# Optimization experiments

Measured on AMD Instinct MI355X. Metric: run time of the kernel, lower is better.

## Reference

```python
import jax, jax.numpy as jnp
from jax import lax
import numpy as np

N_HOS, N_TYPES, N_STRUCTS = 4, 16, 512
N_COMBOS = N_HOS * N_TYPES  # 64
HID = 1024
N_ITERS = 60  # fixed PDHG iterations (differentiable unrolled solver)


def setup_inputs() -> dict:
    key = jax.random.key(0)
    ks = jax.random.split(key, 8)
    X = jax.random.uniform(ks[0], (2048, N_HOS, N_TYPES), dtype=jnp.float32)
    # sparse 0/1 structure matrix; guarantee each structure touches >=1 combo
    S = (jax.random.uniform(ks[1], (N_COMBOS, N_STRUCTS)) < 0.08).astype(jnp.float32)
    cols = jnp.arange(N_STRUCTS)
    S = S.at[cols % N_COMBOS, cols].set(1.0)
    # MLP params (He-ish init)
    W1 = jax.random.normal(ks[2], (N_COMBOS, HID), dtype=jnp.float32) * (2.0 / N_COMBOS) ** 0.5
    b1 = jnp.zeros((HID,), jnp.float32)
    W2 = jax.random.normal(ks[3], (HID, HID), dtype=jnp.float32) * (2.0 / HID) ** 0.5
    b2 = jnp.zeros((HID,), jnp.float32)
    W3 = jax.random.normal(ks[4], (HID, N_STRUCTS), dtype=jnp.float32) * (2.0 / HID) ** 0.5
    b3 = jnp.zeros((N_STRUCTS,), jnp.float32)
    return {"X": X, "W1": W1, "b1": b1, "W2": W2, "b2": b2,
            "W3": W3, "b3": b3, "S": S, "batch_size": 2048}


def nn_forward(X, W1, b1, W2, b2, W3, b3):
    # torch loop applies act_fun after EVERY layer, including the last
    Z = X.reshape(X.shape[0], -1)                 # [B, n_hos*n_types]
    Z = jax.nn.relu(Z @ W1 + b1)
    Z = jax.nn.relu(Z @ W2 + b2)
    Z = jax.nn.relu(Z @ W3 + b3)                  # [B, n_structures]
    return Z


def solve_lp(S, W, B, Z, n_iters=N_ITERS):
    """Batched solve of: max_x W.x - ||x - Z||_2  s.t. x >= 0, S x <= B.
    PDHG (Chambolle-Pock) on  min_x f(x) + i{Kx <= c},
    f(x) = -W.x + ||x - Z||_2,  K = [S; -I],  c = [B; 0].
    Same optimization problem as the CvxpyLayer, solved by a fixed-iteration
    batched primal-dual method (differentiable via unrolling)."""
    batch, n = Z.shape
    m = S.shape[0]

    # ||K||_2 via power iteration on K^T K = S^T S + I (constant wrt params)
    def pow_step(v, _):
        v2 = S.T @ (S @ v) + v
        return v2 / jnp.linalg.norm(v2), None
    v0 = jnp.full((n,), 1.0 / np.sqrt(n), Z.dtype)
    v, _ = lax.scan(pow_step, v0, None, length=30)
    L = jnp.sqrt(jnp.vdot(v, S.T @ (S @ v) + v))
    L = lax.stop_gradient(L)
    tau = 0.9 / L
    sigma = 0.9 / L

    c = jnp.concatenate([B, jnp.zeros_like(Z)], axis=-1)  # [B, m+n]

    def Kx(x):
        return jnp.concatenate([x @ S.T, -x], axis=-1)    # [B, m+n]

    def KTy(y):
        return y[:, :m] @ S - y[:, m:]                    # [B, n]

    def prox_f(v):
        # argmin_x 1/(2 tau) ||x - v||^2 - W.x + ||x - Z||_2
        u = v + tau * W
        d = u - Z
        nrm = jnp.linalg.norm(d, axis=-1, keepdims=True)
        scale = jnp.maximum(1.0 - tau / jnp.maximum(nrm, 1e-12), 0.0)
        return Z + scale * d

    def step(carry, _):
        x, xbar, y = carry
        y = jnp.maximum(y + sigma * (Kx(xbar) - c), 0.0)
        x_new = prox_f(x - tau * KTy(y))
        xbar = 2.0 * x_new - x
        return (x_new, xbar, y), None

    x0 = jnp.zeros_like(Z)
    y0 = jnp.zeros((batch, m + n), Z.dtype)
    (x, _, _), _ = lax.scan(step, (x0, x0, y0), None, length=n_iters)
    return x


def reference(X, W1, b1, W2, b2, W3, b3, S, batch_size):
    Z = nn_forward(X, W1, b1, W2, b2, W3, b3)     # [B, n_structures]
    W = jnp.ones_like(Z)                          # weights w = 1 (as in torch)
    B = X.reshape(batch_size, -1)                 # capacities b
    return solve_lp(S, W, B, Z)
```

## Files before the change

kernel.cpp:

```cpp
#include <hip/hip_runtime.h>


typedef _Float16 half8 __attribute__((ext_vector_type(8)));
typedef __fp16 fp16x2 __attribute__((ext_vector_type(2)));
typedef __fp16 fp16x4 __attribute__((ext_vector_type(4)));
typedef float floatx4 __attribute__((ext_vector_type(4)));
typedef float floatx2 __attribute__((ext_vector_type(2)));

#define BATCH 2048
#define NITERS 60
#define XBS 520
#define YLS 72

typedef const __attribute__((address_space(1))) unsigned int* gptr_as1;
typedef __attribute__((address_space(3))) unsigned int* lptr_as3;
__device__ __forceinline__ void gl_lds16(const _Float16* g, _Float16* s) {
    __builtin_amdgcn_global_load_lds((gptr_as1)g, (lptr_as3)s, 16, 0, 0);
}

template <int CTRL>
__device__ __forceinline__ float dpp_addf(float x) {
    int y = __builtin_amdgcn_update_dpp(0, __builtin_bit_cast(int, x), CTRL, 0xf, 0xf, true);
    return x + __builtin_bit_cast(float, y);
}
__device__ __forceinline__ float sum16(float x) {
    x = dpp_addf<0xB1>(x);
    x = dpp_addf<0x4E>(x);
    x = dpp_addf<0x124>(x);
    x = dpp_addf<0x128>(x);
    return x;
}
__device__ __forceinline__ float sum64(float x) {
    x = sum16(x);
    x += __builtin_bit_cast(float, __builtin_amdgcn_ds_swizzle(__builtin_bit_cast(int, x), 0x401F));
    x += __shfl_xor(x, 32, 64);
    return x;
}

__device__ void power_64(const float* __restrict__ S, float* __restrict__ tau_g) {
    __shared__ unsigned long long rowm[64][8];
    __shared__ float G[64][65];
    __shared__ float wl[64], pg[4][64];
    int t = threadIdx.x, wv = t >> 6, ln = t & 63;
    for (int rr = 0; rr < 16; rr++) {
        int r = wv * 16 + rr;
        float v[8];
#pragma unroll
        for (int e = 0; e < 8; e++) v[e] = S[r * 512 + e * 64 + ln];
#pragma unroll
        for (int e = 0; e < 8; e++) {
            unsigned long long m = __ballot(v[e] != 0.f);
            if (ln == 0) rowm[r][e] = m;
        }
    }
    __syncthreads();
    for (int k = 0; k < 16; k++) {
        int idx = t * 16 + k;
        int i = idx >> 6, j = idx & 63;
        int cnt = 0;
#pragma unroll
        for (int e = 0; e < 8; e++) cnt += __popcll(rowm[i][e] & rowm[j][e]);
        G[i][j] = (float)cnt;
    }
    if (wv == 0) {
        int cnt = 0;
#pragma unroll
        for (int e = 0; e < 8; e++) cnt += __popcll(rowm[ln][e]);
        wl[ln] = (float)cnt * 0.044194173824159216f;
    }
    __syncthreads();
    for (int s = 0; s < 30; s++) {
        float a = 0.f;
#pragma unroll
        for (int jj = 0; jj < 16; jj++) {
            int j = wv * 16 + jj;
            a += G[ln][j] * wl[j];
        }
        pg[wv][ln] = a;
        __syncthreads();
        if (wv == 0) {
            float g = (pg[0][ln] + pg[1][ln]) + (pg[2][ln] + pg[3][ln]);
            float wi = wl[ln];
            float s1 = sum64(wi * g);
            float s2 = sum64(wi * wi);
            float n = sqrtf(s1 + 2.f * s2 + 1.f);
            wl[ln] = (g + wi) / n;
        }
        __syncthreads();
    }
    if (wv == 0) {
        float wi = wl[ln];
        float s2 = sum64(wi * wi);
        if (ln == 0) tau_g[0] = 0.9f / sqrtf(s2 + 1.f);
    }
}

__global__ __launch_bounds__(256) void prep(
    const float* __restrict__ X, _Float16* __restrict__ Xh,
    const float* __restrict__ W1, _Float16* __restrict__ W1t,
    const float* __restrict__ W2, _Float16* __restrict__ W2t,
    const float* __restrict__ W3, _Float16* __restrict__ W3t,
    const float* __restrict__ S, _Float16* __restrict__ s1f,
    _Float16* __restrict__ s2f) {
    __shared__ float tile[32][33];
    int tid = threadIdx.x;
    int bid = blockIdx.x;
    if (bid < 512) {
        int i = bid * 256 + tid;
        Xh[i] = (_Float16)X[i];
        return;
    }
    bid -= 512;
    if (bid < 1600) {
        const float* W; _Float16* Wt; int K, N, b;
        if (bid < 64)        { W = W1; Wt = W1t; K = 64;   N = 1024; b = bid; }
        else if (bid < 1088) { W = W2; Wt = W2t; K = 1024; N = 1024; b = bid - 64; }
        else                 { W = W3; Wt = W3t; K = 1024; N = 512;  b = bid - 1088; }
        int nbx = N / 32;
        int n0 = (b % nbx) * 32, k0 = (b / nbx) * 32;
        int tx = tid & 31, ty = tid >> 5;
#pragma unroll
        for (int i = 0; i < 4; i++)
            tile[ty + i * 8][tx] = W[(size_t)(k0 + ty + i * 8) * N + n0 + tx];
        __syncthreads();
#pragma unroll
        for (int i = 0; i < 4; i++)
            Wt[(size_t)(n0 + ty + i * 8) * K + k0 + tx] = (_Float16)tile[tx][ty + i * 8];
        return;
    }
    bid -= 1600;
    int i = bid * 256 + tid;
    if (i < 4 * 16 * 64 * 8) {
        int j = i & 7, lane = (i >> 3) & 63, kk = (i >> 9) & 15, wc = i >> 13;
        int pos = kk * 32 + (lane >> 4) * 8 + j;
        int pp = pos >> 7, r = pos & 127;
        int hh = r >> 6, r2 = r & 63;
        int lmc = r2 >> 2, t3 = r2 & 3;
        int c = pp * 128 + (hh * 4 + t3) * 16 + lmc;
        int m = wc * 16 + (lane & 15);
        s1f[i] = (_Float16)S[m * 512 + c];
    } else {
        int i2 = i - 4 * 16 * 64 * 8;
        int j = i2 & 7, lane = (i2 >> 3) & 63, c = (i2 >> 9) & 1,
            tt = (i2 >> 10) & 7, wc = i2 >> 13;
        int kc = c * 32 + (lane >> 4) * 8 + j;
        int n = wc * 128 + tt * 16 + (lane & 15);
        s2f[i2] = (_Float16)S[kc * 512 + n];
    }
}

__global__ __launch_bounds__(256) void gemm_relu(
    const _Float16* __restrict__ A, const _Float16* __restrict__ Wt,
    const float* __restrict__ bias, _Float16* __restrict__ outh,
    float* __restrict__ outf, int N, int K,
    const float* __restrict__ Sp, float* __restrict__ tau_g) {
    __shared__ __align__(16) _Float16 As[128 * 32];
    __shared__ __align__(16) _Float16 Bs[64 * 32];
    int tid = threadIdx.x;
    int bm = blockIdx.y * 128;
    int bn = blockIdx.x * 64;
    if (bn >= N) {
        if (blockIdx.y == 0 && Sp) power_64(Sp, tau_g);
        return;
    }
    int w = tid >> 6, l = tid & 63;
    int wr = w >> 1, wc = w & 1;
    int lm = l & 15, q = l >> 4;
    floatx4 acc[4][2] = {};

    int sr = l >> 2;
    int sc = (l & 3) * 8;
    const _Float16* ag0 = A + (size_t)(bm + w * 32 + sr) * K + sc;
    const _Float16* ag1 = A + (size_t)(bm + w * 32 + 16 + sr) * K + sc;
    _Float16* as0 = &As[(w * 32) * 32];
    _Float16* as1 = &As[(w * 32 + 16) * 32];
    const _Float16* bg = Wt + (size_t)(bn + w * 16 + sr) * K + sc;
    _Float16* bs = &Bs[(w * 16) * 32];

    for (int k0 = 0; k0 < K; k0 += 32) {
        gl_lds16(ag0 + k0, as0);
        gl_lds16(ag1 + k0, as1);
        gl_lds16(bg + k0, bs);
        __syncthreads();
        half8 af[4], bf[2];
#pragma unroll
        for (int mt = 0; mt < 4; mt++)
            af[mt] = *(const half8*)&As[(wr * 64 + mt * 16 + lm) * 32 + q * 8];
#pragma unroll
        for (int nt = 0; nt < 2; nt++)
            bf[nt] = *(const half8*)&Bs[(wc * 32 + nt * 16 + lm) * 32 + q * 8];
#pragma unroll
        for (int mt = 0; mt < 4; mt++)
#pragma unroll
            for (int nt = 0; nt < 2; nt++)
                acc[mt][nt] = __builtin_amdgcn_mfma_f32_16x16x32_f16(
                    af[mt], bf[nt], acc[mt][nt], 0, 0, 0);
        __syncthreads();
    }
#pragma unroll
    for (int nt = 0; nt < 2; nt++) {
        int col = bn + wc * 32 + nt * 16 + lm;
        float bv = bias[col];
#pragma unroll
        for (int mt = 0; mt < 4; mt++) {
#pragma unroll
            for (int v = 0; v < 4; v++) {
                int row = bm + wr * 64 + mt * 16 + q * 4 + v;
                float val = fmaxf(acc[mt][nt][v] + bv, 0.f);
                if (outh) outh[(size_t)row * N + col] = (_Float16)val;
                else      outf[(size_t)row * N + col] = val;
            }
        }
    }
}

__global__ __launch_bounds__(256, 1) void pdhg_mfma(
    const float* __restrict__ Zb, const float* __restrict__ Xf,
    const _Float16* __restrict__ s1f, const _Float16* __restrict__ s2f,
    const float* __restrict__ tau_p, float* __restrict__ out) {
    __shared__ __align__(16) _Float16 xb_d[8 * XBS];
    __shared__ __align__(16) _Float16 yl_d[8 * YLS];
    __shared__ __align__(16) float red[8][4];
    int tid = threadIdx.x;
    int p = tid >> 6;
    int l = tid & 63, lm = l & 15, q = l >> 4;
    int lq = lm & 7;
    int qa = q & 1;
    int h = q >> 1;
    int b0 = blockIdx.x * 8;

    half8 s1[16], s2[8][2];
#pragma unroll
    for (int k = 0; k < 16; k++)
        s1[k] = *(const half8*)&s1f[((p * 16 + k) * 64 + l) * 8];
#pragma unroll
    for (int u = 0; u < 8; u++)
#pragma unroll
        for (int c = 0; c < 2; c++)
            s2[u][c] = *(const half8*)&s2f[(((p * 8 + u) * 2 + c) * 64 + l) * 8];

    floatx4 z4[4], tz4[4], x4[4], xb4[4], yh4[4], d4[4];
    floatx4 ylo = {}, Bc;
    floatx4 a1p[4] = {};
    floatx4 acc2[8] = {};
    const floatx4 zero4 = {0.f, 0.f, 0.f, 0.f};
    float tau = tau_p[0];
    float sig = tau;

#pragma unroll
    for (int v = 0; v < 4; v++)
        Bc[v] = Xf[(b0 + qa * 4 + v) * 64 + p * 16 + lm];
#pragma unroll
    for (int t = 0; t < 4; t++) {
#pragma unroll
        for (int v = 0; v < 4; v++) {
            float zz = Zb[(size_t)(b0 + qa * 4 + v) * 512 + p * 128 + (h * 4 + t) * 16 + lm];
            z4[t][v] = zz;
            tz4[t][v] = tau - zz;
        }
        x4[t] = zero4; xb4[t] = zero4; yh4[t] = zero4;
    }
    {
        half8 hz = {0, 0, 0, 0, 0, 0, 0, 0};
        for (int i = tid; i < (8 * XBS) / 8; i += 256)
            *(half8*)&xb_d[i * 8] = hz;
        for (int i = tid; i < 8 * YLS; i += 256)
            yl_d[i] = (_Float16)0.f;
    }
    __syncthreads();

#pragma unroll 1
    for (int it = 0; it < NITERS; ++it) {
#pragma unroll
        for (int k = 0; k < 16; k++) {
            half8 ad = *(const half8*)&xb_d[lq * XBS + k * 32 + q * 8];
            a1p[k & 3] = __builtin_amdgcn_mfma_f32_16x16x32_f16(ad, s1[k], a1p[k & 3], 0, 0, 0);
        }
        floatx4 a1 = (a1p[0] + a1p[1]) + (a1p[2] + a1p[3]);
        floatx4 yv = __builtin_elementwise_max(ylo + sig * (a1 - Bc), zero4);
        floatx4 dy = yv - ylo;
        ylo = yv;
        if (q < 2) {
#pragma unroll
            for (int v = 0; v < 4; v++)
                yl_d[(q * 4 + v) * YLS + p * 16 + lm] = (_Float16)dy[v];
        }
        __syncthreads();
        half8 a2d[2];
#pragma unroll
        for (int c = 0; c < 2; c++)
            a2d[c] = *(const half8*)&yl_d[lq * YLS + c * 32 + q * 8];
#pragma unroll
        for (int u = 0; u < 8; u++)
#pragma unroll
            for (int c = 0; c < 2; c++)
                acc2[u] = __builtin_amdgcn_mfma_f32_16x16x32_f16(a2d[c], s2[u][c], acc2[u], 0, 0, 0);
        floatx4 pn = {};
#pragma unroll
        for (int t = 0; t < 4; t++) {
            floatx4 accs = h ? acc2[t + 4] : acc2[t];
            yh4[t] = __builtin_elementwise_max(yh4[t] - sig * xb4[t], zero4);
            floatx4 kty = accs - yh4[t];
            floatx4 dd = (x4[t] - tau * kty) + tz4[t];
            d4[t] = dd;
            pn += dd * dd;
        }
#pragma unroll
        for (int v = 0; v < 4; v++) pn[v] = sum16(pn[v]);
#pragma unroll
        for (int v = 0; v < 4; v++) pn[v] += __shfl_xor(pn[v], 32, 64);
        if (lm == 0 && q < 2) {
#pragma unroll
            for (int v = 0; v < 4; v++) red[q * 4 + v][p] = pn[v];
        }
        __syncthreads();
        floatx4 sv;
#pragma unroll
        for (int v = 0; v < 4; v++) {
            floatx4 rr = *(const floatx4*)&red[qa * 4 + v][0];
            float n2 = (rr.x + rr.y) + (rr.z + rr.w);
            sv[v] = fmaxf(1.f - tau * rsqrtf(fmaxf(n2, 1e-24f)), 0.f);
        }
#pragma unroll
        for (int t = 0; t < 4; t++) {
            floatx4 xn = z4[t] + sv * d4[t];
            floatx4 xbn = 2.f * xn - x4[t];
            d4[t] = xbn - xb4[t];
            x4[t] = xn;
            xb4[t] = xbn;
        }
#pragma unroll
        for (int v = 0; v < 4; v++) {
            fp16x2 p0 = __builtin_amdgcn_cvt_pkrtz(d4[0][v], d4[1][v]);
            fp16x2 p1 = __builtin_amdgcn_cvt_pkrtz(d4[2][v], d4[3][v]);
            fp16x4 hd = __builtin_shufflevector(p0, p1, 0, 1, 2, 3);
            *(fp16x4*)&xb_d[(qa * 4 + v) * XBS + p * 128 + h * 64 + lm * 4] = hd;
        }
        __syncthreads();
    }
#pragma unroll
    for (int t = 0; t < 4; t++)
#pragma unroll
        for (int v = 0; v < 4; v++)
            out[(size_t)(b0 + qa * 4 + v) * 512 + p * 128 + (h * 4 + t) * 16 + lm] = x4[t][v];
}

extern "C" void kernel_launch(void* const* d_in, const int* in_sizes, int n_in,
                              void* d_out, int out_size, void* d_ws, size_t ws_size,
                              hipStream_t stream) {
    const float* X  = (const float*)d_in[0];
    const float* W1 = (const float*)d_in[1];
    const float* b1 = (const float*)d_in[2];
    const float* W2 = (const float*)d_in[3];
    const float* b2 = (const float*)d_in[4];
    const float* W3 = (const float*)d_in[5];
    const float* b3 = (const float*)d_in[6];
    const float* S  = (const float*)d_in[7];
    float* out = (float*)d_out;

    char* ws = (char*)d_ws;
    size_t off = 0;
    auto alloc = [&](size_t bytes) {
        void* p = ws + off;
        off += (bytes + 255) & ~(size_t)255;
        return p;
    };
    _Float16* Xh  = (_Float16*)alloc((size_t)BATCH * 64 * 2);
    _Float16* W1t = (_Float16*)alloc((size_t)64 * 1024 * 2);
    _Float16* W2t = (_Float16*)alloc((size_t)1024 * 1024 * 2);
    _Float16* W3t = (_Float16*)alloc((size_t)1024 * 512 * 2);
    _Float16* H1  = (_Float16*)alloc((size_t)BATCH * 1024 * 2);
    _Float16* H2  = (_Float16*)alloc((size_t)BATCH * 1024 * 2);
    float*    Zb  = (float*)alloc((size_t)BATCH * 512 * 4);
    _Float16* s1f = (_Float16*)alloc((size_t)4 * 16 * 64 * 8 * 2);
    _Float16* s2f = (_Float16*)alloc((size_t)4 * 8 * 2 * 64 * 8 * 2);
    float*    tau = (float*)alloc(256);

    hipLaunchKernelGGL(prep, dim3(2368), dim3(256), 0, stream,
                       X, Xh, W1, W1t, W2, W2t, W3, W3t, S, s1f, s2f);
    hipLaunchKernelGGL(gemm_relu, dim3(16, 16), dim3(256), 0, stream,
                       Xh, W1t, b1, H1, (float*)nullptr, 1024, 64,
                       (const float*)nullptr, (float*)nullptr);
    hipLaunchKernelGGL(gemm_relu, dim3(17, 16), dim3(256), 0, stream,
                       H1, W2t, b2, H2, (float*)nullptr, 1024, 1024, S, tau);
    hipLaunchKernelGGL(gemm_relu, dim3(8, 16), dim3(256), 0, stream,
                       H2, W3t, b3, (_Float16*)nullptr, Zb, 512, 1024,
                       (const float*)nullptr, (float*)nullptr);
    hipLaunchKernelGGL(pdhg_mfma, dim3(BATCH / 8), dim3(256), 0, stream,
                       Zb, X, s1f, s2f, tau, out);
}
```

Measured before the change: 208.2 us.

## Defer xbar update into next iteration to drop a per-iteration barrier

The x/xbar update after the norm reduction moves to the start of the next iteration. Before the reduction barrier, each thread writes two fp16 LDS buffers, u1 = (z-x)+(z-xbar) and d. The next iteration rebuilds the xbar delta as u1 + 2*sv*d in fp16 just before the MFMAs. This removes one of the three __syncthreads per PDHG iteration. In exchange it doubles the LDS reads and writes for that operand and adds packed fp16 arithmetic, which may add rounding error.

New measurement: 234.3 us. 1.13x slower.

```diff
diff --git a/kernel.cpp b/kernel.cpp
--- a/kernel.cpp
+++ b/kernel.cpp
@@ -218,15 +218,15 @@
     const float* __restrict__ Zb, const float* __restrict__ Xf,
     const _Float16* __restrict__ s1f, const _Float16* __restrict__ s2f,
     const float* __restrict__ tau_p, float* __restrict__ out) {
-    __shared__ __align__(16) _Float16 xb_d[8 * XBS];
+    __shared__ __align__(16) _Float16 u1_d[8 * XBS];
+    __shared__ __align__(16) _Float16 dd_d[8 * XBS];
     __shared__ __align__(16) _Float16 yl_d[8 * YLS];
     __shared__ __align__(16) float red[8][4];
     int tid = threadIdx.x;
     int p = tid >> 6;
     int l = tid & 63, lm = l & 15, q = l >> 4;
     int lq = lm & 7;
-    int qa = q & 1;
-    int h = q >> 1;
+    int qa = q & 1, h = q >> 1;
     int b0 = blockIdx.x * 8;
 
     half8 s1[16], s2[8][2];
@@ -258,23 +258,46 @@
             z4[t][v] = zz;
             tz4[t][v] = tau - zz;
         }
-        x4[t] = zero4; xb4[t] = zero4; yh4[t] = zero4;
+        x4[t] = zero4; xb4[t] = zero4; yh4[t] = zero4; d4[t] = zero4;
     }
     {
         half8 hz = {0, 0, 0, 0, 0, 0, 0, 0};
-        for (int i = tid; i < (8 * XBS) / 8; i += 256)
-            *(half8*)&xb_d[i * 8] = hz;
-        for (int i = tid; i < 8 * YLS; i += 256)
-            yl_d[i] = (_Float16)0.f;
+        for (int i = tid; i < (8 * XBS) / 8; i += 256) {
+            *(half8*)&u1_d[i * 8] = hz;
+            *(half8*)&dd_d[i * 8] = hz;
+        }
+        if (tid < 32) ((float*)red)[tid] = 0.f;
     }
     __syncthreads();
 
 #pragma unroll 1
     for (int it = 0; it < NITERS; ++it) {
+        floatx4 rra = *(const floatx4*)&red[lq][0];
+        float n2a = (rra.x + rra.y) + (rra.z + rra.w);
+        float sva = fmaxf(1.f - tau * rsqrtf(fmaxf(n2a, 1e-24f)), 0.f);
+        _Float16 svh = (_Float16)(2.f * sva);
+        half8 svb = {svh, svh, svh, svh, svh, svh, svh, svh};
+        if (it) {
+            floatx4 sv4;
+#pragma unroll
+            for (int v = 0; v < 4; v++) {
+                floatx4 rr = *(const floatx4*)&red[qa * 4 + v][0];
+                float n2 = (rr.x + rr.y) + (rr.z + rr.w);
+                sv4[v] = fmaxf(1.f - tau * rsqrtf(fmaxf(n2, 1e-24f)), 0.f);
+            }
+#pragma unroll
+            for (int t = 0; t < 4; t++) {
+                floatx4 xn = z4[t] + sv4 * d4[t];
+                xb4[t] = 2.f * xn - x4[t];
+                x4[t] = xn;
+            }
+        }
 #pragma unroll
         for (int k = 0; k < 16; k++) {
-            half8 ad = *(const half8*)&xb_d[lq * XBS + k * 32 + q * 8];
-            a1p[k & 3] = __builtin_amdgcn_mfma_f32_16x16x32_f16(ad, s1[k], a1p[k & 3], 0, 0, 0);
+            half8 uh = *(const half8*)&u1_d[lq * XBS + k * 32 + q * 8];
+            half8 dh = *(const half8*)&dd_d[lq * XBS + k * 32 + q * 8];
+            half8 af = uh + svb * dh;
+            a1p[k & 3] = __builtin_amdgcn_mfma_f32_16x16x32_f16(af, s1[k], a1p[k & 3], 0, 0, 0);
         }
         floatx4 a1 = (a1p[0] + a1p[1]) + (a1p[2] + a1p[3]);
         floatx4 yv = __builtin_elementwise_max(ylo + sig * (a1 - Bc), zero4);
@@ -296,14 +319,24 @@
             for (int c = 0; c < 2; c++)
                 acc2[u] = __builtin_amdgcn_mfma_f32_16x16x32_f16(a2d[c], s2[u][c], acc2[u], 0, 0, 0);
         floatx4 pn = {};
+        floatx4 u1t[4];
 #pragma unroll
         for (int t = 0; t < 4; t++) {
-            floatx4 accs = h ? acc2[t + 4] : acc2[t];
+            floatx4 accs = h ? acc2[4 + t] : acc2[t];
             yh4[t] = __builtin_elementwise_max(yh4[t] - sig * xb4[t], zero4);
             floatx4 kty = accs - yh4[t];
-            floatx4 dd = (x4[t] - tau * kty) + tz4[t];
-            d4[t] = dd;
-            pn += dd * dd;
+            floatx4 ddv = (x4[t] - tau * kty) + tz4[t];
+            d4[t] = ddv;
+            pn += ddv * ddv;
+            u1t[t] = (z4[t] - x4[t]) + (z4[t] - xb4[t]);
+        }
+#pragma unroll
+        for (int v = 0; v < 4; v++) {
+            fp16x4 hu = {(__fp16)u1t[0][v], (__fp16)u1t[1][v], (__fp16)u1t[2][v], (__fp16)u1t[3][v]};
+            fp16x4 hd = {(__fp16)d4[0][v], (__fp16)d4[1][v], (__fp16)d4[2][v], (__fp16)d4[3][v]};
+            int adr = (qa * 4 + v) * XBS + p * 128 + h * 64 + lm * 4;
+            *(fp16x4*)&u1_d[adr] = hu;
+            *(fp16x4*)&dd_d[adr] = hd;
         }
 #pragma unroll
         for (int v = 0; v < 4; v++) pn[v] = sum16(pn[v]);
@@ -314,35 +347,21 @@
             for (int v = 0; v < 4; v++) red[q * 4 + v][p] = pn[v];
         }
         __syncthreads();
-        floatx4 sv;
-#pragma unroll
-        for (int v = 0; v < 4; v++) {
-            floatx4 rr = *(const floatx4*)&red[qa * 4 + v][0];
-            float n2 = (rr.x + rr.y) + (rr.z + rr.w);
-            sv[v] = fmaxf(1.f - tau * rsqrtf(fmaxf(n2, 1e-24f)), 0.f);
-        }
-#pragma unroll
-        for (int t = 0; t < 4; t++) {
-            floatx4 xn = z4[t] + sv * d4[t];
-            floatx4 xbn = 2.f * xn - x4[t];
-            d4[t] = xbn - xb4[t];
-            x4[t] = xn;
-            xb4[t] = xbn;
-        }
-#pragma unroll
-        for (int v = 0; v < 4; v++) {
-            fp16x2 p0 = __builtin_amdgcn_cvt_pkrtz(d4[0][v], d4[1][v]);
-            fp16x2 p1 = __builtin_amdgcn_cvt_pkrtz(d4[2][v], d4[3][v]);
-            fp16x4 hd = __builtin_shufflevector(p0, p1, 0, 1, 2, 3);
-            *(fp16x4*)&xb_d[(qa * 4 + v) * XBS + p * 128 + h * 64 + lm * 4] = hd;
-        }
-        __syncthreads();
-    }
-#pragma unroll
-    for (int t = 0; t < 4; t++)
+    }
+    floatx4 sv4;
+#pragma unroll
+    for (int v = 0; v < 4; v++) {
+        floatx4 rr = *(const floatx4*)&red[qa * 4 + v][0];
+        float n2 = (rr.x + rr.y) + (rr.z + rr.w);
+        sv4[v] = fmaxf(1.f - tau * rsqrtf(fmaxf(n2, 1e-24f)), 0.f);
+    }
+#pragma unroll
+    for (int t = 0; t < 4; t++) {
+        floatx4 xn = z4[t] + sv4 * d4[t];
 #pragma unroll
         for (int v = 0; v < 4; v++)
-            out[(size_t)(b0 + qa * 4 + v) * 512 + p * 128 + (h * 4 + t) * 16 + lm] = x4[t][v];
+            out[(size_t)(b0 + qa * 4 + v) * 512 + p * 128 + (h * 4 + t) * 16 + lm] = xn[v];
+    }
 }
 
 extern "C" void kernel_launch(void* const* d_in, const int* in_sizes, int n_in,
```
